# Kernel tuning notes

Hardware: AMD Instinct MI355X
Metric: run time of the kernel (lower is better)

## Reference

```python
import jax, jax.numpy as jnp
import numpy as np

N = 8  # fixed node count per sample (hardcoded in the torch module)


def setup_inputs() -> dict:
    key = jax.random.key(0)
    ks = jax.random.split(key, 13)
    B = 131072

    def w(k, shape, fan_in):
        # torch nn.Linear default init: U(-1/sqrt(fan_in), 1/sqrt(fan_in))
        return jax.random.uniform(k, shape, jnp.float32, -1.0, 1.0) / np.sqrt(fan_in).astype(np.float32)

    return {
        "x": jax.random.normal(ks[0], (B, N), jnp.float32),
        "enc_w1": w(ks[1], (3, 64), 3),   "enc_b1": w(ks[2], (64,), 3),
        "enc_w2": w(ks[3], (64, 2), 64),  "enc_b2": w(ks[4], (2,), 64),
        "gcn1_w": w(ks[5], (2, 32), 2),   "gcn1_b": w(ks[6], (32,), 2),
        "gcn2_w": w(ks[7], (32, 32), 32), "gcn2_b": w(ks[8], (32,), 32),
        "dec_w1": w(ks[9], (32, 64), 32), "dec_b1": w(ks[10], (64,), 32),
        "dec_w2": w(ks[11], (64, 3), 64), "dec_b2": w(ks[12], (3,), 64),
    }


def _gabriel_norm_adj(p):
    """Batched Gabriel graph -> GCN-normalized (A + I) with unit edge weights.

    p: (B, N, 2) latent 2D points.
    Edge (i,j) exists iff no other point k lies strictly inside the circle
    with diameter (p_i, p_j)  (dist(p_k, mid)^2 < r^2, matching torch's '<').
    Gabriel graphs contain the nearest-neighbor graph, so for N>=2 edges always
    exist and the torch fallback branch is unreachable.
    Returns D^{-1/2} (A + I) D^{-1/2} of shape (B, N, N) (GCNConv default:
    add_self_loops=True with weight 1, symmetric normalization).
    """
    mid = (p[:, :, None, :] + p[:, None, :, :]) * 0.5                 # (B,N,N,2)
    r2 = jnp.sum((p[:, :, None, :] - mid) ** 2, axis=-1)              # (B,N,N)
    # d2[b,i,j,k] = ||p[b,k] - mid[b,i,j]||^2  -> (B,N,N,N), the big intermediate
    d2 = jnp.sum((p[:, None, None, :, :] - mid[:, :, :, None, :]) ** 2, axis=-1)
    a = jnp.arange(N)
    k_not_ij = (a[None, None, :] != a[:, None, None]) & (a[None, None, :] != a[None, :, None])  # (N,N,N) [i,j,k]
    blocked = jnp.any((d2 < r2[..., None]) & k_not_ij, axis=-1)       # (B,N,N)
    off_diag = a[:, None] != a[None, :]
    adj = ((~blocked) & off_diag).astype(p.dtype)                     # symmetric Gabriel adjacency
    a_hat = adj + jnp.eye(N, dtype=p.dtype)                           # self-loops, weight 1
    dinv = jax.lax.rsqrt(jnp.sum(a_hat, axis=-1))                     # (B,N)
    return dinv[:, :, None] * a_hat * dinv[:, None, :]


def reference(x, enc_w1, enc_b1, enc_w2, enc_b2,
              gcn1_w, gcn1_b, gcn2_w, gcn2_b,
              dec_w1, dec_b1, dec_w2, dec_b2):
    B = x.shape[0]
    idx = jnp.arange(N, dtype=x.dtype)
    # preprocess: (B, N, 3) rows [0, value, index]
    xp = jnp.stack([jnp.zeros_like(x), x, jnp.broadcast_to(idx, x.shape)], axis=-1)
    latent = jax.nn.relu(xp @ enc_w1 + enc_b1) @ enc_w2 + enc_b2      # (B,N,2)
    # torch builds the graph from detach().cpu().numpy() -> no grad through structure
    norm = jax.lax.stop_gradient(_gabriel_norm_adj(latent))           # (B,N,N)
    h1 = jax.nn.relu(jnp.einsum('bij,bjf->bif', norm, latent @ gcn1_w) + gcn1_b)  # (B,N,32)
    h2 = jnp.einsum('bij,bjf->bif', norm, h1 @ gcn2_w) + gcn2_b                    # (B,N,32)
    pooled = jnp.mean(h2, axis=1)                                     # (B,32)
    node = jnp.broadcast_to(pooled[:, None, :], (B, N, pooled.shape[-1]))
    dec = jax.nn.relu(node @ dec_w1 + dec_b1) @ dec_w2 + dec_b2       # (B,N,3)
    reconstructed = dec[:, :, 1]                                      # (B,N)
    return reconstructed, latent
```

## Files before the change

### kernel.cpp

```cpp
#include <hip/hip_runtime.h>


typedef float v2 __attribute__((ext_vector_type(2)));
static __device__ __forceinline__ v2 sp(float s) { return (v2){s, s}; }
static __device__ __forceinline__ v2 fma2(v2 a, v2 b, v2 c) {
    return __builtin_elementwise_fma(a, b, c);
}
static __device__ __forceinline__ v2 ldv2(const float* p) {
    return *reinterpret_cast<const v2*>(p);
}

template <int I, int J>
static __device__ __forceinline__ void gpair(const v2* __restrict__ p,
                                             unsigned& ml, unsigned& mh)
{
    #pragma clang fp contract(off)
    v2 mid = (p[I] + p[J]) * sp(0.5f);
    v2 di = p[I] - mid;  v2 si = di * di;  float r2i = si.x + si.y;
    v2 dj = p[J] - mid;  v2 sj = dj * dj;  float r2j = sj.x + sj.y;
    float dmin = 3.4e38f;
    #pragma unroll
    for (int k = 0; k < 8; ++k) {
        if (k == I || k == J) continue;
        v2 dk = p[k] - mid;
        v2 sk = dk * dk;
        dmin = fminf(dmin, sk.x + sk.y);
    }
    constexpr unsigned bi = 1u << (((I & 3) * 8) + J);
    constexpr unsigned bj = 1u << (((J & 3) * 8) + I);
    if (I < 4) ml |= (dmin < r2i) ? 0u : bi; else mh |= (dmin < r2i) ? 0u : bi;
    if (J < 4) ml |= (dmin < r2j) ? 0u : bj; else mh |= (dmin < r2j) ? 0u : bj;
}

__global__ __launch_bounds__(256, 8) void gae_main(
    const float* __restrict__ x,
    const float* __restrict__ enc_w1,
    const float* __restrict__ enc_b1,
    const float* __restrict__ enc_w2,
    const float* __restrict__ enc_b2,
    const float* __restrict__ gcn1_w,
    const float* __restrict__ gcn1_b,
    const float* __restrict__ gcn2_w,
    const float* __restrict__ gcn2_b,
    const float* __restrict__ dec_w1,
    const float* __restrict__ dec_b1,
    const float* __restrict__ dec_w2,
    const float* __restrict__ dec_b2,
    float* __restrict__ out_rec,
    float* __restrict__ out_lat,
    int B)
{
    __shared__ __align__(16) float smem[4096];
    v2*       const A2 = reinterpret_cast<v2*>(smem);
    unsigned* const MB = reinterpret_cast<unsigned*>(smem + 2048);
    v2*       const N2 = reinterpret_cast<v2*>(smem + 2560);
    float*    const CJ = smem + 3584;
    float*    const PL = smem + 2048;
    float*    const OO = smem;

    const int lane = threadIdx.x & 63;
    const int ru   = __builtin_amdgcn_readfirstlane(threadIdx.x >> 6);
    int g = blockIdx.x * 64 + lane;
    if (g >= B) g = B - 1;

    const float2 xr = *reinterpret_cast<const float2*>(x + (size_t)g * 8 + 2 * ru);
    const v2 xp2 = (v2){xr.x, xr.y};
    const float i0f = (float)(2 * ru), i1f = i0f + 1.0f;

    v2 pl0, pl1;
    { const v2 b2v = ldv2(enc_b2); pl0 = b2v; pl1 = b2v; }
    #pragma unroll 8
    for (int h = 0; h < 64; ++h) {
        const float wx = enc_w1[64 + h];
        const float wi = enc_w1[128 + h];
        const float bb = enc_b1[h];
        const v2 uxy = ldv2(enc_w2 + 2 * h);
        const float c0 = fmaf(i0f, wi, bb);
        const float c1 = fmaf(i1f, wi, bb);
        v2 t = fma2(xp2, sp(wx), (v2){c0, c1});
        float t0 = fmaxf(t.x, 0.0f);
        float t1 = fmaxf(t.y, 0.0f);
        pl0 = fma2(sp(t0), uxy, pl0);
        pl1 = fma2(sp(t1), uxy, pl1);
    }

    A2[(2 * ru + 0) * 64 + lane] = pl0;
    A2[(2 * ru + 1) * 64 + lane] = pl1;
    __syncthreads();
    v2 p[8];
    #pragma unroll
    for (int j = 0; j < 8; ++j) p[j] = A2[j * 64 + lane];

    unsigned ml = 0u, mh = 0u;
    if (ru == 0) {
        gpair<0,1>(p, ml, mh); gpair<0,2>(p, ml, mh); gpair<0,3>(p, ml, mh);
        gpair<0,4>(p, ml, mh); gpair<0,5>(p, ml, mh); gpair<0,6>(p, ml, mh);
        gpair<0,7>(p, ml, mh);
    } else if (ru == 1) {
        gpair<1,2>(p, ml, mh); gpair<1,3>(p, ml, mh); gpair<1,4>(p, ml, mh);
        gpair<1,5>(p, ml, mh); gpair<1,6>(p, ml, mh); gpair<1,7>(p, ml, mh);
        gpair<2,3>(p, ml, mh);
    } else if (ru == 2) {
        gpair<2,4>(p, ml, mh); gpair<2,5>(p, ml, mh); gpair<2,6>(p, ml, mh);
        gpair<2,7>(p, ml, mh); gpair<3,4>(p, ml, mh); gpair<3,5>(p, ml, mh);
        gpair<3,6>(p, ml, mh);
    } else {
        gpair<3,7>(p, ml, mh); gpair<4,5>(p, ml, mh); gpair<4,6>(p, ml, mh);
        gpair<4,7>(p, ml, mh); gpair<5,6>(p, ml, mh); gpair<5,7>(p, ml, mh);
        gpair<6,7>(p, ml, mh);
    }

    MB[ru * 128 +  0 + lane] = ml;
    MB[ru * 128 + 64 + lane] = mh;
    __syncthreads();
    ml = (MB[0 * 128 + lane] | MB[1 * 128 + lane]) |
         (MB[2 * 128 + lane] | MB[3 * 128 + lane]) | 0x08040201u;
    mh = (MB[0 * 128 + 64 + lane] | MB[1 * 128 + 64 + lane]) |
         (MB[2 * 128 + 64 + lane] | MB[3 * 128 + 64 + lane]) | 0x80402010u;

    float dinv[8];
    v2 q[8];
    #pragma unroll
    for (int i = 0; i < 8; ++i) {
        const unsigned rb = ((i < 4 ? ml : mh) >> ((i & 3) * 8)) & 0xffu;
        dinv[i] = __builtin_amdgcn_rsqf((float)__popc(rb));
        q[i] = sp(dinv[i]) * p[i];
    }

    {
        const unsigned w = (ru < 2) ? ml : mh;
        const int sh = ((2 * ru) & 3) * 8;
        const unsigned rb0 = (w >> sh) & 0xffu;
        const unsigned rb1 = (w >> (sh + 8)) & 0xffu;
        const float dv0 = __builtin_amdgcn_rsqf((float)__popc(rb0));
        const float dv1 = __builtin_amdgcn_rsqf((float)__popc(rb1));
        v2 a0 = sp(0.0f), a1 = sp(0.0f);
        #pragma unroll
        for (int j = 0; j < 8; ++j) {
            a0 = fma2(sp((float)((rb0 >> j) & 1u)), q[j], a0);
            a1 = fma2(sp((float)((rb1 >> j) & 1u)), q[j], a1);
        }
        N2[(2 * ru + 0) * 64 + lane] = sp(dv0) * a0;
        N2[(2 * ru + 1) * 64 + lane] = sp(dv1) * a1;

        const int j0 = 2 * ru, j1 = 2 * ru + 1;
        float s0 = 0.0f, s1 = 0.0f;
        #pragma unroll
        for (int i = 0; i < 8; ++i) {
            const unsigned rb = ((i < 4 ? ml : mh) >> ((i & 3) * 8)) & 0xffu;
            s0 = fmaf((float)((rb >> j0) & 1u), dinv[i], s0);
            s1 = fmaf((float)((rb >> j1) & 1u), dinv[i], s1);
        }
        CJ[j0 * 64 + lane] = 0.125f * dv0 * s0;
        CJ[j1 * 64 + lane] = 0.125f * dv1 * s1;
    }
    __syncthreads();

    const float* w0 = gcn1_w + 8 * ru;
    const float* w1 = gcn1_w + 32 + 8 * ru;
    const float* bl = gcn1_b + 8 * ru;
    v2 t2[4];
    #pragma unroll
    for (int fp = 0; fp < 4; ++fp) t2[fp] = sp(0.0f);
    #pragma unroll
    for (int i = 0; i < 8; ++i) {
        const v2 ni = N2[i * 64 + lane];
        const float ci = CJ[i * 64 + lane];
        const v2 nxi = sp(ni.x), nyi = sp(ni.y), civ = sp(ci);
        #pragma unroll
        for (int fp = 0; fp < 4; ++fp) {
            v2 h = fma2(nxi, ldv2(w0 + 2 * fp),
                   fma2(nyi, ldv2(w1 + 2 * fp), ldv2(bl + 2 * fp)));
            h = __builtin_elementwise_max(h, sp(0.0f));
            t2[fp] = fma2(civ, h, t2[fp]);
        }
    }

    #pragma unroll
    for (int fp = 0; fp < 4; ++fp) A2[(4 * ru + fp) * 64 + lane] = t2[fp];
    __syncthreads();

    v2 pg2[4];
    #pragma unroll
    for (int kp = 0; kp < 4; ++kp) pg2[kp] = ldv2(gcn2_b + 8 * ru + 2 * kp);
    #pragma unroll
    for (int fp = 0; fp < 16; ++fp) {
        const v2 tv = A2[fp * 64 + lane];
        #pragma unroll
        for (int half = 0; half < 2; ++half) {
            const int f = 2 * fp + half;
            const v2 tf = sp(half ? tv.y : tv.x);
            const float* wr = gcn2_w + f * 32 + 8 * ru;
            #pragma unroll
            for (int kp = 0; kp < 4; ++kp)
                pg2[kp] = fma2(tf, ldv2(wr + 2 * kp), pg2[kp]);
        }
    }
    #pragma unroll
    for (int kp = 0; kp < 4; ++kp) {
        PL[(8 * ru + 2 * kp + 0) * 64 + lane] = pg2[kp].x;
        PL[(8 * ru + 2 * kp + 1) * 64 + lane] = pg2[kp].y;
    }
    __syncthreads();

    const float* db = dec_b1 + 16 * ru;
    v2 a2[8];
    #pragma unroll
    for (int hp = 0; hp < 8; ++hp) a2[hp] = ldv2(db + 2 * hp);
    __builtin_amdgcn_s_setprio(1);
    #pragma unroll
    for (int f = 0; f < 32; ++f) {
        const float pf = PL[f * 64 + lane];
        const v2 pfv = sp(pf);
        const float* wr = dec_w1 + f * 64 + 16 * ru;
        #pragma unroll
        for (int hp = 0; hp < 8; ++hp)
            a2[hp] = fma2(pfv, ldv2(wr + 2 * hp), a2[hp]);
    }
    __builtin_amdgcn_s_setprio(0);
    v2 oacc = sp(0.0f);
    #pragma unroll
    for (int hp = 0; hp < 8; ++hp) {
        v2 rr = __builtin_elementwise_max(a2[hp], sp(0.0f));
        const int h0 = 16 * ru + 2 * hp;
        const v2 wv = (v2){dec_w2[h0 * 3 + 1], dec_w2[h0 * 3 + 4]};
        oacc = fma2(rr, wv, oacc);
    }
    const float opart = oacc.x + oacc.y;

    OO[ru * 64 + lane] = opart;
    __syncthreads();
    const float outv = ((OO[lane] + OO[64 + lane]) +
                        (OO[128 + lane] + OO[192 + lane])) + dec_b2[1];

    *reinterpret_cast<float4*>(out_lat + (size_t)g * 16 + 4 * ru) =
        make_float4(pl0.x, pl0.y, pl1.x, pl1.y);
    *reinterpret_cast<float2*>(out_rec + (size_t)g * 8 + 2 * ru) =
        make_float2(outv, outv);
}

extern "C" void kernel_launch(void* const* d_in, const int* in_sizes, int n_in,
                              void* d_out, int out_size, void* d_ws, size_t ws_size,
                              hipStream_t stream) {
    const float* x       = (const float*)d_in[0];
    const float* enc_w1  = (const float*)d_in[1];
    const float* enc_b1  = (const float*)d_in[2];
    const float* enc_w2  = (const float*)d_in[3];
    const float* enc_b2  = (const float*)d_in[4];
    const float* gcn1_w  = (const float*)d_in[5];
    const float* gcn1_b  = (const float*)d_in[6];
    const float* gcn2_w  = (const float*)d_in[7];
    const float* gcn2_b  = (const float*)d_in[8];
    const float* dec_w1  = (const float*)d_in[9];
    const float* dec_b1  = (const float*)d_in[10];
    const float* dec_w2  = (const float*)d_in[11];
    const float* dec_b2  = (const float*)d_in[12];

    const int B = in_sizes[0] / 8;
    float* out_rec = (float*)d_out;
    float* out_lat = out_rec + (size_t)B * 8;
    (void)d_ws; (void)ws_size;

    const int blocks = (B + 63) / 64;
    gae_main<<<blocks, 256, 0, stream>>>(
        x, enc_w1, enc_b1, enc_w2, enc_b2,
        gcn1_w, gcn1_b, gcn2_w, gcn2_b,
        dec_w1, dec_b1, dec_w2, dec_b2,
        out_rec, out_lat, B);
}
```

Baseline: 106.1 us.

## Split each sample across eight wavefronts instead of four

The block grows from 256 to 512 threads, so each of the eight wavefronts handles one node and a 1/8 share of the feature dimensions, where previously four wavefronts handled two nodes each. Per-thread work and register pressure drop, and the 28 Gabriel pair tests are rebalanced across eight waves. In exchange the encoder weight loads are duplicated across more waves, the bitmask and pooling reductions read eight partials, and the output stores become narrower. Shared memory regions are re-laid out to fit.

```diff
diff --git a/kernel.cpp b/kernel.cpp
--- a/kernel.cpp
+++ b/kernel.cpp
@@ -32,7 +32,7 @@
     if (J < 4) ml |= (dmin < r2j) ? 0u : bj; else mh |= (dmin < r2j) ? 0u : bj;
 }
 
-__global__ __launch_bounds__(256, 8) void gae_main(
+__global__ __launch_bounds__(512, 8) void gae_main(
     const float* __restrict__ x,
     const float* __restrict__ enc_w1,
     const float* __restrict__ enc_b1,
@@ -51,10 +51,11 @@
     int B)
 {
     __shared__ __align__(16) float smem[4096];
-    v2*       const A2 = reinterpret_cast<v2*>(smem);
-    unsigned* const MB = reinterpret_cast<unsigned*>(smem + 2048);
-    v2*       const N2 = reinterpret_cast<v2*>(smem + 2560);
-    float*    const CJ = smem + 3584;
+    v2*       const P2 = reinterpret_cast<v2*>(smem);
+    unsigned* const MB = reinterpret_cast<unsigned*>(smem + 1024);
+    v2*       const N2 = reinterpret_cast<v2*>(smem + 2048);
+    float*    const CJ = smem + 3072;
+    v2*       const T2 = reinterpret_cast<v2*>(smem);
     float*    const PL = smem + 2048;
     float*    const OO = smem;
 
@@ -63,60 +64,58 @@
     int g = blockIdx.x * 64 + lane;
     if (g >= B) g = B - 1;
 
-    const float2 xr = *reinterpret_cast<const float2*>(x + (size_t)g * 8 + 2 * ru);
-    const v2 xp2 = (v2){xr.x, xr.y};
-    const float i0f = (float)(2 * ru), i1f = i0f + 1.0f;
-
-    v2 pl0, pl1;
-    { const v2 b2v = ldv2(enc_b2); pl0 = b2v; pl1 = b2v; }
+    const float xi = x[(size_t)g * 8 + ru];
+    const float ifl = (float)ru;
+
+    v2 pl = ldv2(enc_b2);
     #pragma unroll 8
     for (int h = 0; h < 64; ++h) {
         const float wx = enc_w1[64 + h];
         const float wi = enc_w1[128 + h];
         const float bb = enc_b1[h];
         const v2 uxy = ldv2(enc_w2 + 2 * h);
-        const float c0 = fmaf(i0f, wi, bb);
-        const float c1 = fmaf(i1f, wi, bb);
-        v2 t = fma2(xp2, sp(wx), (v2){c0, c1});
-        float t0 = fmaxf(t.x, 0.0f);
-        float t1 = fmaxf(t.y, 0.0f);
-        pl0 = fma2(sp(t0), uxy, pl0);
-        pl1 = fma2(sp(t1), uxy, pl1);
-    }
-
-    A2[(2 * ru + 0) * 64 + lane] = pl0;
-    A2[(2 * ru + 1) * 64 + lane] = pl1;
+        float t = fmaf(xi, wx, fmaf(ifl, wi, bb));
+        t = fmaxf(t, 0.0f);
+        pl = fma2(sp(t), uxy, pl);
+    }
+
+    P2[ru * 64 + lane] = pl;
     __syncthreads();
     v2 p[8];
     #pragma unroll
-    for (int j = 0; j < 8; ++j) p[j] = A2[j * 64 + lane];
+    for (int j = 0; j < 8; ++j) p[j] = P2[j * 64 + lane];
 
     unsigned ml = 0u, mh = 0u;
-    if (ru == 0) {
-        gpair<0,1>(p, ml, mh); gpair<0,2>(p, ml, mh); gpair<0,3>(p, ml, mh);
-        gpair<0,4>(p, ml, mh); gpair<0,5>(p, ml, mh); gpair<0,6>(p, ml, mh);
-        gpair<0,7>(p, ml, mh);
-    } else if (ru == 1) {
-        gpair<1,2>(p, ml, mh); gpair<1,3>(p, ml, mh); gpair<1,4>(p, ml, mh);
-        gpair<1,5>(p, ml, mh); gpair<1,6>(p, ml, mh); gpair<1,7>(p, ml, mh);
-        gpair<2,3>(p, ml, mh);
-    } else if (ru == 2) {
-        gpair<2,4>(p, ml, mh); gpair<2,5>(p, ml, mh); gpair<2,6>(p, ml, mh);
-        gpair<2,7>(p, ml, mh); gpair<3,4>(p, ml, mh); gpair<3,5>(p, ml, mh);
-        gpair<3,6>(p, ml, mh);
-    } else {
-        gpair<3,7>(p, ml, mh); gpair<4,5>(p, ml, mh); gpair<4,6>(p, ml, mh);
-        gpair<4,7>(p, ml, mh); gpair<5,6>(p, ml, mh); gpair<5,7>(p, ml, mh);
-        gpair<6,7>(p, ml, mh);
-    }
+    if      (ru == 0) { gpair<0,1>(p, ml, mh); gpair<0,2>(p, ml, mh);
+                        gpair<0,3>(p, ml, mh); gpair<0,4>(p, ml, mh); }
+    else if (ru == 1) { gpair<0,5>(p, ml, mh); gpair<0,6>(p, ml, mh);
+                        gpair<0,7>(p, ml, mh); gpair<1,2>(p, ml, mh); }
+    else if (ru == 2) { gpair<1,3>(p, ml, mh); gpair<1,4>(p, ml, mh);
+                        gpair<1,5>(p, ml, mh); gpair<1,6>(p, ml, mh); }
+    else if (ru == 3) { gpair<1,7>(p, ml, mh); gpair<2,3>(p, ml, mh);
+                        gpair<2,4>(p, ml, mh); gpair<2,5>(p, ml, mh); }
+    else if (ru == 4) { gpair<2,6>(p, ml, mh); gpair<2,7>(p, ml, mh);
+                        gpair<3,4>(p, ml, mh); }
+    else if (ru == 5) { gpair<3,5>(p, ml, mh); gpair<3,6>(p, ml, mh);
+                        gpair<3,7>(p, ml, mh); }
+    else if (ru == 6) { gpair<4,5>(p, ml, mh); gpair<4,6>(p, ml, mh);
+                        gpair<4,7>(p, ml, mh); }
+    else              { gpair<5,6>(p, ml, mh); gpair<5,7>(p, ml, mh);
+                        gpair<6,7>(p, ml, mh); }
 
     MB[ru * 128 +  0 + lane] = ml;
     MB[ru * 128 + 64 + lane] = mh;
     __syncthreads();
-    ml = (MB[0 * 128 + lane] | MB[1 * 128 + lane]) |
-         (MB[2 * 128 + lane] | MB[3 * 128 + lane]) | 0x08040201u;
-    mh = (MB[0 * 128 + 64 + lane] | MB[1 * 128 + 64 + lane]) |
-         (MB[2 * 128 + 64 + lane] | MB[3 * 128 + 64 + lane]) | 0x80402010u;
+    {
+        unsigned al = 0u, ah = 0u;
+        #pragma unroll
+        for (int r = 0; r < 8; ++r) {
+            al |= MB[r * 128 + lane];
+            ah |= MB[r * 128 + 64 + lane];
+        }
+        ml = al | 0x08040201u;
+        mh = ah | 0x80402010u;
+    }
 
     float dinv[8];
     v2 q[8];
@@ -128,47 +127,37 @@
     }
 
     {
-        const unsigned w = (ru < 2) ? ml : mh;
-        const int sh = ((2 * ru) & 3) * 8;
-        const unsigned rb0 = (w >> sh) & 0xffu;
-        const unsigned rb1 = (w >> (sh + 8)) & 0xffu;
-        const float dv0 = __builtin_amdgcn_rsqf((float)__popc(rb0));
-        const float dv1 = __builtin_amdgcn_rsqf((float)__popc(rb1));
-        v2 a0 = sp(0.0f), a1 = sp(0.0f);
-        #pragma unroll
-        for (int j = 0; j < 8; ++j) {
-            a0 = fma2(sp((float)((rb0 >> j) & 1u)), q[j], a0);
-            a1 = fma2(sp((float)((rb1 >> j) & 1u)), q[j], a1);
-        }
-        N2[(2 * ru + 0) * 64 + lane] = sp(dv0) * a0;
-        N2[(2 * ru + 1) * 64 + lane] = sp(dv1) * a1;
-
-        const int j0 = 2 * ru, j1 = 2 * ru + 1;
-        float s0 = 0.0f, s1 = 0.0f;
+        const unsigned w = (ru < 4) ? ml : mh;
+        const unsigned rb = (w >> ((ru & 3) * 8)) & 0xffu;
+        const float dv = __builtin_amdgcn_rsqf((float)__popc(rb));
+        v2 a = sp(0.0f);
+        #pragma unroll
+        for (int j = 0; j < 8; ++j)
+            a = fma2(sp((float)((rb >> j) & 1u)), q[j], a);
+        N2[ru * 64 + lane] = sp(dv) * a;
+
+        float s = 0.0f;
         #pragma unroll
         for (int i = 0; i < 8; ++i) {
-            const unsigned rb = ((i < 4 ? ml : mh) >> ((i & 3) * 8)) & 0xffu;
-            s0 = fmaf((float)((rb >> j0) & 1u), dinv[i], s0);
-            s1 = fmaf((float)((rb >> j1) & 1u), dinv[i], s1);
-        }
-        CJ[j0 * 64 + lane] = 0.125f * dv0 * s0;
-        CJ[j1 * 64 + lane] = 0.125f * dv1 * s1;
-    }
-    __syncthreads();
-
-    const float* w0 = gcn1_w + 8 * ru;
-    const float* w1 = gcn1_w + 32 + 8 * ru;
-    const float* bl = gcn1_b + 8 * ru;
-    v2 t2[4];
-    #pragma unroll
-    for (int fp = 0; fp < 4; ++fp) t2[fp] = sp(0.0f);
+            const unsigned ri = ((i < 4 ? ml : mh) >> ((i & 3) * 8)) & 0xffu;
+            s = fmaf((float)((ri >> ru) & 1u), dinv[i], s);
+        }
+        CJ[ru * 64 + lane] = 0.125f * dv * s;
+    }
+    __syncthreads();
+
+    const float* w0 = gcn1_w + 4 * ru;
+    const float* w1 = gcn1_w + 32 + 4 * ru;
+    const float* bl = gcn1_b + 4 * ru;
+    v2 t2[2];
+    t2[0] = sp(0.0f); t2[1] = sp(0.0f);
     #pragma unroll
     for (int i = 0; i < 8; ++i) {
         const v2 ni = N2[i * 64 + lane];
         const float ci = CJ[i * 64 + lane];
         const v2 nxi = sp(ni.x), nyi = sp(ni.y), civ = sp(ci);
         #pragma unroll
-        for (int fp = 0; fp < 4; ++fp) {
+        for (int fp = 0; fp < 2; ++fp) {
             v2 h = fma2(nxi, ldv2(w0 + 2 * fp),
                    fma2(nyi, ldv2(w1 + 2 * fp), ldv2(bl + 2 * fp)));
             h = __builtin_elementwise_max(h, sp(0.0f));
@@ -176,53 +165,50 @@
         }
     }
 
-    #pragma unroll
-    for (int fp = 0; fp < 4; ++fp) A2[(4 * ru + fp) * 64 + lane] = t2[fp];
-    __syncthreads();
-
-    v2 pg2[4];
-    #pragma unroll
-    for (int kp = 0; kp < 4; ++kp) pg2[kp] = ldv2(gcn2_b + 8 * ru + 2 * kp);
+    T2[(2 * ru + 0) * 64 + lane] = t2[0];
+    T2[(2 * ru + 1) * 64 + lane] = t2[1];
+    __syncthreads();
+
+    v2 pg2[2];
+    pg2[0] = ldv2(gcn2_b + 4 * ru);
+    pg2[1] = ldv2(gcn2_b + 4 * ru + 2);
     #pragma unroll
     for (int fp = 0; fp < 16; ++fp) {
-        const v2 tv = A2[fp * 64 + lane];
+        const v2 tv = T2[fp * 64 + lane];
         #pragma unroll
         for (int half = 0; half < 2; ++half) {
             const int f = 2 * fp + half;
             const v2 tf = sp(half ? tv.y : tv.x);
-            const float* wr = gcn2_w + f * 32 + 8 * ru;
-            #pragma unroll
-            for (int kp = 0; kp < 4; ++kp)
-                pg2[kp] = fma2(tf, ldv2(wr + 2 * kp), pg2[kp]);
-        }
-    }
-    #pragma unroll
-    for (int kp = 0; kp < 4; ++kp) {
-        PL[(8 * ru + 2 * kp + 0) * 64 + lane] = pg2[kp].x;
-        PL[(8 * ru + 2 * kp + 1) * 64 + lane] = pg2[kp].y;
-    }
-    __syncthreads();
-
-    const float* db = dec_b1 + 16 * ru;
-    v2 a2[8];
-    #pragma unroll
-    for (int hp = 0; hp < 8; ++hp) a2[hp] = ldv2(db + 2 * hp);
+            const float* wr = gcn2_w + f * 32 + 4 * ru;
+            pg2[0] = fma2(tf, ldv2(wr + 0), pg2[0]);
+            pg2[1] = fma2(tf, ldv2(wr + 2), pg2[1]);
+        }
+    }
+    PL[(4 * ru + 0) * 64 + lane] = pg2[0].x;
+    PL[(4 * ru + 1) * 64 + lane] = pg2[0].y;
+    PL[(4 * ru + 2) * 64 + lane] = pg2[1].x;
+    PL[(4 * ru + 3) * 64 + lane] = pg2[1].y;
+    __syncthreads();
+
+    const float* db = dec_b1 + 8 * ru;
+    v2 a2[4];
+    #pragma unroll
+    for (int hp = 0; hp < 4; ++hp) a2[hp] = ldv2(db + 2 * hp);
     __builtin_amdgcn_s_setprio(1);
     #pragma unroll
     for (int f = 0; f < 32; ++f) {
-        const float pf = PL[f * 64 + lane];
-        const v2 pfv = sp(pf);
-        const float* wr = dec_w1 + f * 64 + 16 * ru;
-        #pragma unroll
-        for (int hp = 0; hp < 8; ++hp)
+        const v2 pfv = sp(PL[f * 64 + lane]);
+        const float* wr = dec_w1 + f * 64 + 8 * ru;
+        #pragma unroll
+        for (int hp = 0; hp < 4; ++hp)
             a2[hp] = fma2(pfv, ldv2(wr + 2 * hp), a2[hp]);
     }
     __builtin_amdgcn_s_setprio(0);
     v2 oacc = sp(0.0f);
     #pragma unroll
-    for (int hp = 0; hp < 8; ++hp) {
+    for (int hp = 0; hp < 4; ++hp) {
         v2 rr = __builtin_elementwise_max(a2[hp], sp(0.0f));
-        const int h0 = 16 * ru + 2 * hp;
+        const int h0 = 8 * ru + 2 * hp;
         const v2 wv = (v2){dec_w2[h0 * 3 + 1], dec_w2[h0 * 3 + 4]};
         oacc = fma2(rr, wv, oacc);
     }
@@ -230,13 +216,15 @@
 
     OO[ru * 64 + lane] = opart;
     __syncthreads();
-    const float outv = ((OO[lane] + OO[64 + lane]) +
-                        (OO[128 + lane] + OO[192 + lane])) + dec_b2[1];
-
-    *reinterpret_cast<float4*>(out_lat + (size_t)g * 16 + 4 * ru) =
-        make_float4(pl0.x, pl0.y, pl1.x, pl1.y);
-    *reinterpret_cast<float2*>(out_rec + (size_t)g * 8 + 2 * ru) =
-        make_float2(outv, outv);
+    const float outv =
+        (((OO[0 * 64 + lane] + OO[1 * 64 + lane]) +
+          (OO[2 * 64 + lane] + OO[3 * 64 + lane])) +
+         ((OO[4 * 64 + lane] + OO[5 * 64 + lane]) +
+          (OO[6 * 64 + lane] + OO[7 * 64 + lane]))) + dec_b2[1];
+
+    *reinterpret_cast<float2*>(out_lat + (size_t)g * 16 + 2 * ru) =
+        make_float2(pl.x, pl.y);
+    out_rec[(size_t)g * 8 + ru] = outv;
 }
 
 extern "C" void kernel_launch(void* const* d_in, const int* in_sizes, int n_in,
@@ -262,7 +250,7 @@
     (void)d_ws; (void)ws_size;
 
     const int blocks = (B + 63) / 64;
-    gae_main<<<blocks, 256, 0, stream>>>(
+    gae_main<<<blocks, 512, 0, stream>>>(
         x, enc_w1, enc_b1, enc_w2, enc_b2,
         gcn1_w, gcn1_b, gcn2_w, gcn2_b,
         dec_w1, dec_b1, dec_w2, dec_b2,
```

Measured after the change: 110.9 us. 1.05x slower.
